# Kernel tuning notes

Measured on AMD Instinct MI355X. Metric: run time of the kernel, lower is better.

## Reference

```python
import jax, jax.numpy as jnp
import numpy as np
from jax import lax

ALPHA = 0.1
HIDDEN_DIM = 512


def setup_inputs() -> dict:
    key = jax.random.key(0)
    ks = jax.random.split(key, 8)
    B, T, I, H, O, R = 64, 1024, 128, 512, 512, 2
    x = jax.random.normal(ks[0], (B, T, I), dtype=jnp.float32)
    h0 = jnp.zeros((B, H), dtype=jnp.float32)
    Wxh = jax.random.normal(ks[1], (H, I), dtype=jnp.float32) / np.sqrt(I)
    bxh = jax.random.normal(ks[2], (H,), dtype=jnp.float32) * 0.01
    U = jax.random.normal(ks[3], (H, R), dtype=jnp.float32) / np.sqrt(H)
    V = jax.random.normal(ks[4], (H, R), dtype=jnp.float32) / np.sqrt(H)
    Why = jax.random.normal(ks[5], (O, H), dtype=jnp.float32) / np.sqrt(H)
    bhy = jax.random.normal(ks[6], (O,), dtype=jnp.float32) * 0.01
    return {"x": x, "h0": h0, "Wxh": Wxh, "bxh": bxh, "U": U, "V": V,
            "Why": Why, "bhy": bhy}


def reference(x, h0, Wxh, bxh, U, V, Why, bhy):
    # x: (B,T,I); precompute the input projection for all timesteps at once
    xproj = jnp.einsum('bti,hi->bth', x, Wxh) + bxh  # (B,T,H)

    def step(h, xp_t):
        # low-rank recurrent map: h @ V @ U.T / hidden_dim
        pre = xp_t + (h @ V) @ U.T / HIDDEN_DIM  # (B,H)
        h_new = (1.0 - ALPHA) * h + ALPHA * jnp.tanh(pre)
        return h_new, h_new

    _, hs = lax.scan(step, h0, jnp.swapaxes(xproj, 0, 1))  # hs: (T,B,H)
    h_all = jnp.swapaxes(hs, 0, 1)  # (B,T,H)
    y = jnp.einsum('bth,oh->bto', h_all, Why) + bhy  # (B,T,O)
    return y, h_all
```

## Files before the change

kernel.cpp:

```cpp
#include <hip/hip_runtime.h>
#include <hip/hip_bf16.h>
#include <cstdint>

#define B_ 64
#define T_ 1024
#define I_ 128
#define H_ 512
#define O_ 512

#define CHUNK_L 32
#define NCHUNK (T_ / CHUNK_L)
#define WARM_ 96

typedef short bf16x8 __attribute__((ext_vector_type(8)));
typedef float f32x4 __attribute__((ext_vector_type(4)));

typedef const __attribute__((address_space(1))) void* gptr_t;
typedef __attribute__((address_space(3))) void* lptr_t;

__device__ __forceinline__ unsigned short f2bf(float f) {
    unsigned int u = __float_as_uint(f);
    u += 0x7fffu + ((u >> 16) & 1u);
    return (unsigned short)(u >> 16);
}
__device__ __forceinline__ float bf2f(unsigned short b) {
    return __uint_as_float(((unsigned int)b) << 16);
}
__device__ __forceinline__ float fast_tanh(float x) {
    float e = __builtin_amdgcn_exp2f(x * 2.8853900817779268f);
    return 1.0f - 2.0f * __builtin_amdgcn_rcpf(e + 1.0f);
}

template <int CTRL>
__device__ __forceinline__ float dpp_add(float v) {
    int t = __builtin_amdgcn_update_dpp(0, __float_as_int(v), CTRL, 0xf, 0xf, true);
    return v + __int_as_float(t);
}
__device__ __forceinline__ float wave_sum64(float v) {
    v = dpp_add<0x111>(v);
    v = dpp_add<0x112>(v);
    v = dpp_add<0x114>(v);
    v = dpp_add<0x118>(v);
    v = dpp_add<0x142>(v);
    v = dpp_add<0x143>(v);
    return __uint_as_float(__builtin_amdgcn_readlane(__float_as_uint(v), 63));
}

#define NX_ (B_ * T_ * I_)
#define NW_ (H_ * I_)
#define NY_ (O_ * H_)

__global__ __launch_bounds__(256)
void cast_all(const float* __restrict__ x, const float* __restrict__ Wxh,
              const float* __restrict__ Why, unsigned short* __restrict__ xb,
              unsigned short* __restrict__ wb, unsigned short* __restrict__ yb) {
    int i4 = (blockIdx.x * 256 + threadIdx.x) * 4;
    const float* s;
    unsigned short* d;
    int off;
    if (i4 < NX_)             { s = x;   d = xb; off = i4; }
    else if (i4 < NX_ + NW_)  { s = Wxh; d = wb; off = i4 - NX_; }
    else                      { s = Why; d = yb; off = i4 - NX_ - NW_; }
    float4 v = *(const float4*)(s + off);
    ushort4 o;
    o.x = f2bf(v.x); o.y = f2bf(v.y); o.z = f2bf(v.z); o.w = f2bf(v.w);
    *(ushort4*)(d + off) = o;
}

#define CPAD_F32 140
#define CPAD_BF16 136

template <bool STORE_BF16>
__global__ __launch_bounds__(256)
void gemm_bt(const unsigned short* __restrict__ A,
             const unsigned short* __restrict__ Bm,
             const float* __restrict__ bias,
             void* __restrict__ Cout,
             int M, int N, int K) {
    __shared__ __align__(16) unsigned char smem_raw[32768];
    unsigned short* As = (unsigned short*)smem_raw;
    unsigned short* Bs = As + 8192;

    const int tid  = threadIdx.x;
    const int lane = tid & 63;
    const int w    = tid >> 6;
    const int wm   = (w >> 1) * 64;
    const int wn   = (w & 1) * 64;
    const int nblk = N >> 7;
    const int bm   = (int)(blockIdx.x / nblk) << 7;
    const int bn   = (int)(blockIdx.x % nblk) << 7;

    f32x4 acc[4][4] = {};

    const int srow = tid >> 2;
    const int scol = (tid & 3) << 3;
    const unsigned short* gA0 = A  + (size_t)(bm + srow) * K + scol;
    const unsigned short* gA1 = A  + (size_t)(bm + 64 + srow) * K + scol;
    const unsigned short* gB0 = Bm + (size_t)(bn + srow) * K + scol;
    const unsigned short* gB1 = Bm + (size_t)(bn + 64 + srow) * K + scol;

    unsigned short* ldsA0 = As + w * 512;
    unsigned short* ldsA1 = As + 2048 + w * 512;
    unsigned short* ldsB0 = Bs + w * 512;
    unsigned short* ldsB1 = Bs + 2048 + w * 512;

    const int frow = lane & 15;
    const int fk   = (lane >> 4) << 3;
    const int nk   = K >> 5;

#define STAGE_T(BUF, KT)                                                                          \
    {                                                                                             \
        const int _o = (BUF) * 4096;                                                              \
        __builtin_amdgcn_global_load_lds((gptr_t)(gA0 + (KT)), (lptr_t)(ldsA0 + _o), 16, 0, 0);   \
        __builtin_amdgcn_global_load_lds((gptr_t)(gA1 + (KT)), (lptr_t)(ldsA1 + _o), 16, 0, 0);   \
        __builtin_amdgcn_global_load_lds((gptr_t)(gB0 + (KT)), (lptr_t)(ldsB0 + _o), 16, 0, 0);   \
        __builtin_amdgcn_global_load_lds((gptr_t)(gB1 + (KT)), (lptr_t)(ldsB1 + _o), 16, 0, 0);   \
    }

    STAGE_T(0, 0)
    __syncthreads();

    for (int t = 0; t < nk; ++t) {
        const int cur = t & 1;
        if (t + 1 < nk) STAGE_T(cur ^ 1, (t + 1) << 5)

        const unsigned short* Ab = As + cur * 4096;
        const unsigned short* Bb = Bs + cur * 4096;
        bf16x8 af[4], bf[4];
#pragma unroll
        for (int mt = 0; mt < 4; ++mt)
            af[mt] = *(const bf16x8*)(Ab + (wm + mt * 16 + frow) * 32 + fk);
#pragma unroll
        for (int nt = 0; nt < 4; ++nt)
            bf[nt] = *(const bf16x8*)(Bb + (wn + nt * 16 + frow) * 32 + fk);
#pragma unroll
        for (int mt = 0; mt < 4; ++mt)
#pragma unroll
            for (int nt = 0; nt < 4; ++nt)
                acc[mt][nt] = __builtin_amdgcn_mfma_f32_16x16x32_bf16(
                    af[mt], bf[nt], acc[mt][nt], 0, 0, 0);

        __syncthreads();
    }
#undef STAGE_T

    const int c_col = lane & 15;
    const int c_row = (lane >> 4) << 2;
    const int slab  = (w >> 1) << 4;
    float* cbf = (float*)smem_raw;
    unsigned short* cbh = (unsigned short*)smem_raw;

#pragma unroll
    for (int mt = 0; mt < 4; ++mt) {
        __syncthreads();
        if (STORE_BF16) {
#pragma unroll
            for (int nt = 0; nt < 4; ++nt) {
                const int col = wn + nt * 16 + c_col;
                const float bv = bias[bn + col];
#pragma unroll
                for (int r = 0; r < 4; ++r)
                    cbh[(slab + c_row + r) * CPAD_BF16 + col] = f2bf(acc[mt][nt][r] + bv);
            }
        } else {
#pragma unroll
            for (int nt = 0; nt < 4; ++nt) {
                const int col = wn + nt * 16 + c_col;
                const float bv = bias[bn + col];
#pragma unroll
                for (int r = 0; r < 4; ++r)
                    cbf[(slab + c_row + r) * CPAD_F32 + col] = acc[mt][nt][r] + bv;
            }
        }
        __syncthreads();
        if (STORE_BF16) {
#pragma unroll
            for (int p = 0; p < 2; ++p) {
                const int lrow = (tid >> 4) + p * 16;
                const int colg = (tid & 15) * 8;
                const int grow = bm + (lrow >> 4) * 64 + mt * 16 + (lrow & 15);
                uint4 vv = *(const uint4*)(cbh + lrow * CPAD_BF16 + colg);
                *(uint4*)((unsigned short*)Cout + (size_t)grow * N + bn + colg) = vv;
            }
        } else {
#pragma unroll
            for (int p = 0; p < 4; ++p) {
                const int lrow = (tid >> 5) + p * 8;
                const int col4 = (tid & 31) * 4;
                const int grow = bm + (lrow >> 4) * 64 + mt * 16 + (lrow & 15);
                float4 vv = *(const float4*)(cbf + lrow * CPAD_F32 + col4);
                *(float4*)((float*)Cout + (size_t)grow * N + bn + col4) = vv;
            }
        }
    }
}

__global__ __launch_bounds__(64)
void scan_kernel(const unsigned short* __restrict__ xproj,
                 const float* __restrict__ h0,
                 const float* __restrict__ U,
                 const float* __restrict__ V,
                 float* __restrict__ hall_f32,
                 unsigned short* __restrict__ hall_bf) {
    const int blk = blockIdx.x;
    const int b = blk / NCHUNK;
    const int c = blk % NCHUNK;
    const int t_start = c * CHUNK_L;
    const int t0 = (t_start - WARM_ > 0) ? (t_start - WARM_) : 0;
    const int nwarm = t_start - t0;
    const int NT = nwarm + CHUNK_L;

    const int lane = threadIdx.x;
    const int hbase = lane * 8;

    const float inv_h = 1.0f / (float)H_;
    float h[8], V0[8], V1[8], U0[8], U1[8];
#pragma unroll
    for (int j = 0; j < 8; ++j) {
        V0[j] = V[(hbase + j) * 2 + 0] * inv_h;
        V1[j] = V[(hbase + j) * 2 + 1] * inv_h;
        U0[j] = U[(hbase + j) * 2 + 0];
        U1[j] = U[(hbase + j) * 2 + 1];
    }
    if (t0 == 0) {
#pragma unroll
        for (int j = 0; j < 8; ++j) h[j] = h0[b * H_ + hbase + j];
    } else {
#pragma unroll
        for (int j = 0; j < 8; ++j) h[j] = 0.f;
    }

    const unsigned short* xp = xproj + ((size_t)b * T_ + t0) * H_ + hbase;
    float* ho = hall_f32 + (size_t)b * T_ * H_ + hbase;
    unsigned short* hb = hall_bf + (size_t)b * T_ * H_ + hbase;

    float s0 = 0.f, s1 = 0.f;
    if (t0 == 0) {
        float a0 = 0.f, a1 = 0.f;
#pragma unroll
        for (int j = 0; j < 8; ++j) { a0 += h[j] * V0[j]; a1 += h[j] * V1[j]; }
        s0 = wave_sum64(a0);
        s1 = wave_sum64(a1);
    }

    uint4 xq0, xq1, xq2, xq3;
#define LOADX(DST, IDX)                                                        \
    {                                                                          \
        int _ii = (IDX);                                                       \
        _ii = _ii < NT ? _ii : NT - 1;                                         \
        DST = *(const uint4*)(xp + (size_t)_ii * H_);                          \
    }
    LOADX(xq0, 0)
    LOADX(xq1, 1)
    LOADX(xq2, 2)
    LOADX(xq3, 3)

#define SCAN_SLOT(REG, IDX, DO_STORE)                                          \
    {                                                                          \
        uint4 xc = REG;                                                        \
        LOADX(REG, (IDX) + 4)                                                  \
        float xp8[8];                                                          \
        {                                                                      \
            unsigned int uu[4] = {xc.x, xc.y, xc.z, xc.w};                     \
            _Pragma("unroll")                                                  \
            for (int q = 0; q < 4; ++q) {                                      \
                xp8[2 * q + 0] = bf2f((unsigned short)(uu[q] & 0xffffu));      \
                xp8[2 * q + 1] = bf2f((unsigned short)(uu[q] >> 16));          \
            }                                                                  \
        }                                                                      \
        float g[8];                                                            \
        _Pragma("unroll")                                                      \
        for (int j = 0; j < 8; ++j)                                            \
            g[j] = fast_tanh(xp8[j] + s0 * U0[j] + s1 * U1[j]);                \
        _Pragma("unroll")                                                      \
        for (int j = 0; j < 8; ++j)                                            \
            h[j] = 0.9f * h[j] + 0.1f * g[j];                                  \
        float p0a = 0.f, p0b = 0.f, p1a = 0.f, p1b = 0.f;                      \
        _Pragma("unroll")                                                      \
        for (int j = 0; j < 4; ++j) {                                          \
            p0a += g[j] * V0[j];       p0b += g[j + 4] * V0[j + 4];            \
            p1a += g[j] * V1[j];       p1b += g[j + 4] * V1[j + 4];            \
        }                                                                      \
        float r0 = wave_sum64(p0a + p0b);                                      \
        float r1 = wave_sum64(p1a + p1b);                                      \
        s0 = 0.9f * s0 + 0.1f * r0;                                            \
        s1 = 0.9f * s1 + 0.1f * r1;                                            \
        if (DO_STORE) {                                                        \
            const size_t tt = (size_t)(t0 + (IDX));                            \
            float4 v0 = make_float4(h[0], h[1], h[2], h[3]);                   \
            float4 v1 = make_float4(h[4], h[5], h[6], h[7]);                   \
            *(float4*)(ho + tt * H_ + 0) = v0;                                 \
            *(float4*)(ho + tt * H_ + 4) = v1;                                 \
            uint4 pb;                                                          \
            pb.x = ((unsigned int)f2bf(h[1]) << 16) | f2bf(h[0]);              \
            pb.y = ((unsigned int)f2bf(h[3]) << 16) | f2bf(h[2]);              \
            pb.z = ((unsigned int)f2bf(h[5]) << 16) | f2bf(h[4]);              \
            pb.w = ((unsigned int)f2bf(h[7]) << 16) | f2bf(h[6]);              \
            *(uint4*)(hb + tt * H_) = pb;                                      \
        }                                                                      \
    }

    int I = 0;
    for (; I < nwarm; I += 4) {
        SCAN_SLOT(xq0, I + 0, false)
        SCAN_SLOT(xq1, I + 1, false)
        SCAN_SLOT(xq2, I + 2, false)
        SCAN_SLOT(xq3, I + 3, false)
    }
    for (; I < NT; I += 4) {
        SCAN_SLOT(xq0, I + 0, true)
        SCAN_SLOT(xq1, I + 1, true)
        SCAN_SLOT(xq2, I + 2, true)
        SCAN_SLOT(xq3, I + 3, true)
    }
#undef SCAN_SLOT
#undef LOADX
}

extern "C" void kernel_launch(void* const* d_in, const int* in_sizes, int n_in,
                              void* d_out, int out_size, void* d_ws, size_t ws_size,
                              hipStream_t stream) {
    const float* x   = (const float*)d_in[0];
    const float* h0  = (const float*)d_in[1];
    const float* Wxh = (const float*)d_in[2];
    const float* bxh = (const float*)d_in[3];
    const float* U   = (const float*)d_in[4];
    const float* V   = (const float*)d_in[5];
    const float* Why = (const float*)d_in[6];
    const float* bhy = (const float*)d_in[7];

    float* y    = (float*)d_out;
    float* hall = y + (size_t)B_ * T_ * O_;

    unsigned short* x_bf    = (unsigned short*)d_ws;
    unsigned short* Wxh_bf  = x_bf + (size_t)B_ * T_ * I_;
    unsigned short* Why_bf  = Wxh_bf + (size_t)H_ * I_;
    unsigned short* xp_bf   = Why_bf + (size_t)O_ * H_;
    unsigned short* hall_bf = xp_bf + (size_t)B_ * T_ * H_;

    cast_all<<<(NX_ + NW_ + NY_) / 1024, 256, 0, stream>>>(
        x, Wxh, Why, x_bf, Wxh_bf, Why_bf);

    gemm_bt<true><<<dim3((B_ * T_ / 128) * (H_ / 128)), 256, 0, stream>>>(
        x_bf, Wxh_bf, bxh, xp_bf, B_ * T_, H_, I_);

    scan_kernel<<<B_ * NCHUNK, 64, 0, stream>>>(xp_bf, h0, U, V, hall, hall_bf);

    gemm_bt<false><<<dim3((B_ * T_ / 128) * (O_ / 128)), 256, 0, stream>>>(
        hall_bf, Why_bf, bhy, y, B_ * T_, O_, H_);
}
```

Before: 458.0 us.

## Split scan into compute and store waves via LDS ring, double chunk length

The scan kernel now runs two waves per block. Wave 0 runs the serial recurrence and writes each group of four hidden states into a double-buffered shared-memory ring. Wave 1 converts those states to bf16 and writes both outputs to global memory one group behind, so the stores leave the latency-critical recurrence. The chunk length is also doubled, which halves the blocks and cuts redundant warm-up work per output step. In exchange, every four steps now costs a block-wide barrier, and there is less block-level parallelism.

```diff
diff --git a/kernel.cpp b/kernel.cpp
--- a/kernel.cpp
+++ b/kernel.cpp
@@ -8,7 +8,7 @@
 #define H_ 512
 #define O_ 512
 
-#define CHUNK_L 32
+#define CHUNK_L 64
 #define NCHUNK (T_ / CHUNK_L)
 #define WARM_ 96
 
@@ -195,7 +195,7 @@
     }
 }
 
-__global__ __launch_bounds__(64)
+__global__ __launch_bounds__(128)
 void scan_kernel(const unsigned short* __restrict__ xproj,
                  const float* __restrict__ h0,
                  const float* __restrict__ U,
@@ -209,53 +209,57 @@
     const int t0 = (t_start - WARM_ > 0) ? (t_start - WARM_) : 0;
     const int nwarm = t_start - t0;
     const int NT = nwarm + CHUNK_L;
-
-    const int lane = threadIdx.x;
+    const int E = NT >> 2;
+
+    const int wid  = threadIdx.x >> 6;
+    const int lane = threadIdx.x & 63;
     const int hbase = lane * 8;
+
+    __shared__ __align__(16) float hring[8][H_];
 
     const float inv_h = 1.0f / (float)H_;
     float h[8], V0[8], V1[8], U0[8], U1[8];
-#pragma unroll
-    for (int j = 0; j < 8; ++j) {
-        V0[j] = V[(hbase + j) * 2 + 0] * inv_h;
-        V1[j] = V[(hbase + j) * 2 + 1] * inv_h;
-        U0[j] = U[(hbase + j) * 2 + 0];
-        U1[j] = U[(hbase + j) * 2 + 1];
-    }
-    if (t0 == 0) {
-#pragma unroll
-        for (int j = 0; j < 8; ++j) h[j] = h0[b * H_ + hbase + j];
-    } else {
-#pragma unroll
-        for (int j = 0; j < 8; ++j) h[j] = 0.f;
-    }
-
+    float s0 = 0.f, s1 = 0.f;
+    uint4 xq0, xq1, xq2, xq3;
     const unsigned short* xp = xproj + ((size_t)b * T_ + t0) * H_ + hbase;
+
+    if (wid == 0) {
+#pragma unroll
+        for (int j = 0; j < 8; ++j) {
+            V0[j] = V[(hbase + j) * 2 + 0] * inv_h;
+            V1[j] = V[(hbase + j) * 2 + 1] * inv_h;
+            U0[j] = U[(hbase + j) * 2 + 0];
+            U1[j] = U[(hbase + j) * 2 + 1];
+        }
+        if (t0 == 0) {
+#pragma unroll
+            for (int j = 0; j < 8; ++j) h[j] = h0[b * H_ + hbase + j];
+            float a0 = 0.f, a1 = 0.f;
+#pragma unroll
+            for (int j = 0; j < 8; ++j) { a0 += h[j] * V0[j]; a1 += h[j] * V1[j]; }
+            s0 = wave_sum64(a0);
+            s1 = wave_sum64(a1);
+        } else {
+#pragma unroll
+            for (int j = 0; j < 8; ++j) h[j] = 0.f;
+        }
+        xq0 = *(const uint4*)xp;
+        xq1 = *(const uint4*)(xp + (size_t)(1 < NT ? 1 : NT - 1) * H_);
+        xq2 = *(const uint4*)(xp + (size_t)(2 < NT ? 2 : NT - 1) * H_);
+        xq3 = *(const uint4*)(xp + (size_t)(3 < NT ? 3 : NT - 1) * H_);
+    }
+
     float* ho = hall_f32 + (size_t)b * T_ * H_ + hbase;
     unsigned short* hb = hall_bf + (size_t)b * T_ * H_ + hbase;
 
-    float s0 = 0.f, s1 = 0.f;
-    if (t0 == 0) {
-        float a0 = 0.f, a1 = 0.f;
-#pragma unroll
-        for (int j = 0; j < 8; ++j) { a0 += h[j] * V0[j]; a1 += h[j] * V1[j]; }
-        s0 = wave_sum64(a0);
-        s1 = wave_sum64(a1);
-    }
-
-    uint4 xq0, xq1, xq2, xq3;
 #define LOADX(DST, IDX)                                                        \
     {                                                                          \
         int _ii = (IDX);                                                       \
         _ii = _ii < NT ? _ii : NT - 1;                                         \
         DST = *(const uint4*)(xp + (size_t)_ii * H_);                          \
     }
-    LOADX(xq0, 0)
-    LOADX(xq1, 1)
-    LOADX(xq2, 2)
-    LOADX(xq3, 3)
-
-#define SCAN_SLOT(REG, IDX, DO_STORE)                                          \
+
+#define PSTEP(REG, IDX, SLOT)                                                  \
     {                                                                          \
         uint4 xc = REG;                                                        \
         LOADX(REG, (IDX) + 4)                                                  \
@@ -285,35 +289,42 @@
         float r1 = wave_sum64(p1a + p1b);                                      \
         s0 = 0.9f * s0 + 0.1f * r0;                                            \
         s1 = 0.9f * s1 + 0.1f * r1;                                            \
-        if (DO_STORE) {                                                        \
-            const size_t tt = (size_t)(t0 + (IDX));                            \
-            float4 v0 = make_float4(h[0], h[1], h[2], h[3]);                   \
-            float4 v1 = make_float4(h[4], h[5], h[6], h[7]);                   \
-            *(float4*)(ho + tt * H_ + 0) = v0;                                 \
-            *(float4*)(ho + tt * H_ + 4) = v1;                                 \
-            uint4 pb;                                                          \
-            pb.x = ((unsigned int)f2bf(h[1]) << 16) | f2bf(h[0]);              \
-            pb.y = ((unsigned int)f2bf(h[3]) << 16) | f2bf(h[2]);              \
-            pb.z = ((unsigned int)f2bf(h[5]) << 16) | f2bf(h[4]);              \
-            pb.w = ((unsigned int)f2bf(h[7]) << 16) | f2bf(h[6]);              \
-            *(uint4*)(hb + tt * H_) = pb;                                      \
-        }                                                                      \
-    }
-
-    int I = 0;
-    for (; I < nwarm; I += 4) {
-        SCAN_SLOT(xq0, I + 0, false)
-        SCAN_SLOT(xq1, I + 1, false)
-        SCAN_SLOT(xq2, I + 2, false)
-        SCAN_SLOT(xq3, I + 3, false)
-    }
-    for (; I < NT; I += 4) {
-        SCAN_SLOT(xq0, I + 0, true)
-        SCAN_SLOT(xq1, I + 1, true)
-        SCAN_SLOT(xq2, I + 2, true)
-        SCAN_SLOT(xq3, I + 3, true)
-    }
-#undef SCAN_SLOT
+        *(float4*)(&hring[SLOT][hbase + 0]) = make_float4(h[0], h[1], h[2], h[3]); \
+        *(float4*)(&hring[SLOT][hbase + 4]) = make_float4(h[4], h[5], h[6], h[7]); \
+    }
+
+    for (int e = 0; e <= E; ++e) {
+        if (wid == 0 && e < E) {
+            const int base = 4 * e;
+            const int sb = (e & 1) << 2;
+            PSTEP(xq0, base + 0, sb + 0)
+            PSTEP(xq1, base + 1, sb + 1)
+            PSTEP(xq2, base + 2, sb + 2)
+            PSTEP(xq3, base + 3, sb + 3)
+        }
+        if (wid == 1 && e >= 1) {
+            const int s0i = 4 * (e - 1);
+            if (s0i >= nwarm) {
+                const int sb = ((e - 1) & 1) << 2;
+#pragma unroll
+                for (int k = 0; k < 4; ++k) {
+                    float4 a = *(const float4*)(&hring[sb + k][hbase + 0]);
+                    float4 d = *(const float4*)(&hring[sb + k][hbase + 4]);
+                    const size_t tt = (size_t)(t0 + s0i + k);
+                    *(float4*)(ho + tt * H_ + 0) = a;
+                    *(float4*)(ho + tt * H_ + 4) = d;
+                    uint4 pb;
+                    pb.x = ((unsigned int)f2bf(a.y) << 16) | f2bf(a.x);
+                    pb.y = ((unsigned int)f2bf(a.w) << 16) | f2bf(a.z);
+                    pb.z = ((unsigned int)f2bf(d.y) << 16) | f2bf(d.x);
+                    pb.w = ((unsigned int)f2bf(d.w) << 16) | f2bf(d.z);
+                    *(uint4*)(hb + tt * H_) = pb;
+                }
+            }
+        }
+        __syncthreads();
+    }
+#undef PSTEP
 #undef LOADX
 }
 
@@ -344,7 +355,7 @@
     gemm_bt<true><<<dim3((B_ * T_ / 128) * (H_ / 128)), 256, 0, stream>>>(
         x_bf, Wxh_bf, bxh, xp_bf, B_ * T_, H_, I_);
 
-    scan_kernel<<<B_ * NCHUNK, 64, 0, stream>>>(xp_bf, h0, U, V, hall, hall_bf);
+    scan_kernel<<<B_ * NCHUNK, 128, 0, stream>>>(xp_bf, h0, U, V, hall, hall_bf);
 
     gemm_bt<false><<<dim3((B_ * T_ / 128) * (O_ / 128)), 256, 0, stream>>>(
         hall_bf, Why_bf, bhy, y, B_ * T_, O_, H_);
```

Result: no change. 452.7 us (-1.2%).
